# Kernel tuning notes

Hardware: AMD Instinct MI355X
Metric: run time of the kernel (lower is better)

## Reference

```python
import jax, jax.numpy as jnp
import numpy as np


def _depthwise3x3(x_nhwc, w):
    # w: (3, 3, 1, C) — depthwise conv, padding=1, matches torch Conv2d(groups=C)
    return jax.lax.conv_general_dilated(
        x_nhwc, w, window_strides=(1, 1), padding='SAME',
        dimension_numbers=('NHWC', 'HWIO', 'NHWC'),
        feature_group_count=x_nhwc.shape[-1])


def _stripe_attn(q, k, v, lepe_w, B, H, W, nh, hd, ss, axis, scale):
    # q/k/v: (B, H, W, nh*hd); axis 0 = horizontal stripes, 1 = vertical
    pad_h = (-H) % ss if axis == 0 else 0
    pad_w = (-W) % ss if axis == 1 else 0
    if pad_h or pad_w:
        pad = ((0, 0), (0, pad_h), (0, pad_w), (0, 0))
        q, k, v = jnp.pad(q, pad), jnp.pad(k, pad), jnp.pad(v, pad)
    Hp, Wp = q.shape[1], q.shape[2]
    lepe = _depthwise3x3(v, lepe_w)  # (B, Hp, Wp, nh*hd)

    if axis == 0:
        nS = Hp // ss
        def to_win(t):  # -> (B*nS*Wp, nh, ss, hd)
            t = t.reshape(B, nS, ss, Wp, nh, hd)
            return t.transpose(0, 1, 3, 4, 2, 5).reshape(B * nS * Wp, nh, ss, hd)
    else:
        nS = Wp // ss
        def to_win(t):  # -> (B*Hp*nS, nh, ss, hd)
            t = t.reshape(B, Hp, nS, ss, nh, hd)
            return t.transpose(0, 1, 2, 4, 3, 5).reshape(B * Hp * nS, nh, ss, hd)

    qw, kw, vw, lw = to_win(q), to_win(k), to_win(v), to_win(lepe)
    attn = jax.nn.softmax(jnp.einsum('wnqd,wnkd->wnqk', qw, kw) / scale, axis=-1)
    out = jnp.einsum('wnqk,wnkd->wnqd', attn, vw) + lw  # (Wnum, nh, ss, hd)

    if axis == 0:
        out = out.transpose(0, 2, 1, 3).reshape(B, nS, Wp, ss, nh * hd)
        out = out.transpose(0, 1, 3, 2, 4).reshape(B, Hp, Wp, nh * hd)
    else:
        out = out.transpose(0, 2, 1, 3).reshape(B, Hp, nS, ss, nh * hd)
        out = out.reshape(B, Hp, Wp, nh * hd)
    return out[:, :H, :W, :].reshape(B, H * W, nh * hd)


def setup_inputs() -> dict:
    key = jax.random.key(0)
    ks = jax.random.split(key, 6)
    B, H, W, dim, n_heads, ss = 8, 64, 64, 512, 16, 8
    half = dim // 2
    x = jax.random.normal(ks[0], (B, H * W, dim), dtype=jnp.float32)
    w_qkv = jax.random.normal(ks[1], (3 * dim, dim), dtype=jnp.float32) * 0.02
    w_proj = jax.random.normal(ks[2], (dim, dim), dtype=jnp.float32) * 0.02
    b_proj = jnp.zeros((dim,), dtype=jnp.float32)
    lepe_h_w = jax.random.normal(ks[3], (3, 3, 1, half), dtype=jnp.float32) * 0.1
    lepe_v_w = jax.random.normal(ks[4], (3, 3, 1, half), dtype=jnp.float32) * 0.1
    return {"x": x, "w_qkv": w_qkv, "w_proj": w_proj, "b_proj": b_proj,
            "lepe_h_w": lepe_h_w, "lepe_v_w": lepe_v_w, "H": H, "W": W}


def reference(x, w_qkv, w_proj, b_proj, lepe_h_w, lepe_v_w, H, W):
    B, L, C = x.shape
    n_heads, ss = 16, 8
    hd = C // n_heads
    scale = float(np.sqrt(hd))
    qkv = x @ w_qkv.T  # (B, L, 3C)
    q, k, v = jnp.split(qkv, 3, axis=-1)
    q = q.reshape(B, H, W, C)
    k = k.reshape(B, H, W, C)
    v = v.reshape(B, H, W, C)
    half = C // 2
    nh_h = n_heads // 2
    nh_v = n_heads - nh_h
    out_h = _stripe_attn(q[..., :half], k[..., :half], v[..., :half],
                         lepe_h_w, B, H, W, nh_h, hd, ss, axis=0, scale=scale)
    out_v = _stripe_attn(q[..., half:], k[..., half:], v[..., half:],
                         lepe_v_w, B, H, W, nh_v, hd, ss, axis=1, scale=scale)
    out = jnp.concatenate([out_h, out_v], axis=-1)
    return out @ w_proj.T + b_proj
```

## Files before the change

kernel.cpp:

```cpp
#include <hip/hip_runtime.h>
#include <hip/hip_bf16.h>
#include <stdint.h>

typedef _Float16 half2v __attribute__((ext_vector_type(2)));
typedef _Float16 half8v __attribute__((ext_vector_type(8)));
typedef uint32_t u32x4  __attribute__((ext_vector_type(4)));
typedef float    f32x4  __attribute__((ext_vector_type(4)));

__device__ __forceinline__ unsigned short f2h(float f) {
  _Float16 h = (_Float16)f;
  return __builtin_bit_cast(unsigned short, h);
}
__device__ __forceinline__ half2v bch2(uint32_t u) {
  return __builtin_bit_cast(half2v, u);
}
__device__ __forceinline__ uint32_t pkrtz_u32(float a, float b) {
  return __builtin_bit_cast(uint32_t, __builtin_amdgcn_cvt_pkrtz(a, b));
}

__device__ __forceinline__ int qkv_idx(int half, int b, int n, int h, int w) {
  int idx = half * 8388608 + (b * 8 + n) * 131072;
  idx += (half == 0) ? ((h >> 3) * 16384 + w * 256 + (h & 7) * 32)
                     : (h * 2048 + w * 32);
  return idx;
}

#define GLOAD_LDS16(gsrc, lbase)                                          \
  __builtin_amdgcn_global_load_lds(                                       \
      (const __attribute__((address_space(1))) uint32_t*)(gsrc),          \
      (__attribute__((address_space(3))) uint32_t*)(lbase), 16, 0, 0)

__global__ __launch_bounds__(256) void cvt_f32_f16(const float* __restrict__ in,
                                                   unsigned short* __restrict__ out,
                                                   int n4) {
  int i = blockIdx.x * 256 + threadIdx.x;
  if (i >= n4) return;
  float4 f = reinterpret_cast<const float4*>(in)[i];
  ushort4 u;
  u.x = f2h(f.x); u.y = f2h(f.y); u.z = f2h(f.z); u.w = f2h(f.w);
  reinterpret_cast<ushort4*>(out)[i] = u;
}

template<int MODE>
__global__ __launch_bounds__(512, 2) void gemm_bt(
    const unsigned short* __restrict__ A,
    const unsigned short* __restrict__ B,
    unsigned short* __restrict__ Cq,
    float* __restrict__ Cf,
    const float* __restrict__ bias,
    int M, int N, int K)
{
  __shared__ unsigned short As[4][256 * 32];
  __shared__ unsigned short Bs[4][256 * 32];
  const int tid  = threadIdx.x;
  const int gn   = N >> 8;
  const int cpx  = gridDim.x >> 3;
  const int bid  = blockIdx.x;
  const int wgid = (bid & 7) * cpx + (bid >> 3);
  const int m0   = (wgid / gn) * 256;
  const int n0   = (wgid % gn) * 256;
  const int wave = tid >> 6, lane = tid & 63;
  const int wr  = wave >> 2;
  const int wcn = wave & 3;
  const int sr = tid >> 2;
  const int sc = ((tid & 3) ^ ((tid >> 3) & 3)) * 8;
  const size_t aBase0 = (size_t)(m0 + sr) * K + sc;
  const size_t aBase1 = (size_t)(m0 + 128 + sr) * K + sc;
  const size_t bBase0 = (size_t)(n0 + sr) * K + sc;
  const size_t bBase1 = (size_t)(n0 + 128 + sr) * K + sc;
  char* ldsA = (char*)(&As[0][0]) + (tid & ~63) * 16;
  char* ldsB = (char*)(&Bs[0][0]) + (tid & ~63) * 16;

#define STAGE_TILE(bsel, kofs)                                      \
  do {                                                              \
    GLOAD_LDS16(A + aBase0 + (kofs), ldsA + (bsel) * 16384);        \
    GLOAD_LDS16(A + aBase1 + (kofs), ldsA + (bsel) * 16384 + 8192); \
    GLOAD_LDS16(B + bBase0 + (kofs), ldsB + (bsel) * 16384);        \
    GLOAD_LDS16(B + bBase1 + (kofs), ldsB + (bsel) * 16384 + 8192); \
  } while (0)

  STAGE_TILE(0, 0);
  STAGE_TILE(1, 32);
  STAGE_TILE(2, 64);

  f32x4 acc[8][4];
  const f32x4 zero = {0.f, 0.f, 0.f, 0.f};
  #pragma unroll
  for (int i = 0; i < 8; ++i)
    #pragma unroll
    for (int j = 0; j < 4; ++j) acc[i][j] = zero;

  const int lr   = lane & 15;
  const int slot = (lane >> 4) ^ ((lr >> 1) & 3);

  auto compute = [&](const unsigned short* Asb, const unsigned short* Bsb) {
    half8v bf[4];
    #pragma unroll
    for (int j = 0; j < 4; ++j)
      bf[j] = *reinterpret_cast<const half8v*>(Bsb + (wcn * 64 + j * 16 + lr) * 32 + slot * 8);
    half8v af[8];
    #pragma unroll
    for (int i = 0; i < 8; ++i)
      af[i] = *reinterpret_cast<const half8v*>(Asb + (wr * 128 + i * 16 + lr) * 32 + slot * 8);
    __builtin_amdgcn_s_setprio(1);
    #pragma unroll
    for (int i = 0; i < 8; ++i)
      #pragma unroll
      for (int j = 0; j < 4; ++j)
        acc[i][j] = __builtin_amdgcn_mfma_f32_16x16x32_f16(bf[j], af[i], acc[i][j], 0, 0, 0);
    __builtin_amdgcn_s_setprio(0);
  };

  const int nt = K >> 5;
  for (int t = 0; t < nt; ++t) {
    if (t + 3 < nt) STAGE_TILE((t + 3) & 3, (t + 3) * 32);
    if (t < nt - 3)       asm volatile("s_waitcnt vmcnt(12)" ::: "memory");
    else if (t == nt - 3) asm volatile("s_waitcnt vmcnt(8)"  ::: "memory");
    else if (t == nt - 2) asm volatile("s_waitcnt vmcnt(4)"  ::: "memory");
    else                  asm volatile("s_waitcnt vmcnt(0)"  ::: "memory");
    __builtin_amdgcn_s_barrier();
    __builtin_amdgcn_sched_barrier(0);
    compute(&As[t & 3][0], &Bs[t & 3][0]);
    __builtin_amdgcn_s_barrier();
    __builtin_amdgcn_sched_barrier(0);
  }
#undef STAGE_TILE

  const int cr = (lane >> 4) * 4;
  const int cc = lane & 15;

  if constexpr (MODE == 0) {
    #pragma unroll
    for (int j = 0; j < 4; ++j) {
      const int n = n0 + wcn * 64 + j * 16 + cr;
      const float4 b4 = *reinterpret_cast<const float4*>(bias + n);
      #pragma unroll
      for (int i = 0; i < 8; ++i) {
        const int m = m0 + wr * 128 + i * 16 + cc;
        float4 r;
        r.x = acc[i][j][0] + b4.x;
        r.y = acc[i][j][1] + b4.y;
        r.z = acc[i][j][2] + b4.z;
        r.w = acc[i][j][3] + b4.w;
        *reinterpret_cast<float4*>(Cf + (size_t)m * N + n) = r;
      }
    }
  } else {
    const int mb   = m0 + wr * 128;
    const int btok = mb >> 12;
    const int hr0  = (mb >> 6) & 63;
    #pragma unroll
    for (int j = 0; j < 4; ++j) {
      const int nb    = n0 + wcn * 64 + j * 16 + cr;
      const int tq    = nb >> 9;
      const int halfc = (nb >> 8) & 1;
      const int nn    = (nb & 255) >> 5;
      const int ch4   = nb & 31;
      const int headbase = tq * 16777216 + halfc * 8388608 +
                           (btok * 8 + nn) * 131072 + ch4;
      #pragma unroll
      for (int i = 0; i < 8; ++i) {
        const int hrow = hr0 + (i >> 2);
        const int wpix = (i & 3) * 16 + cc;
        const int off = halfc ? (hrow * 2048 + wpix * 32)
                              : ((hrow >> 3) * 16384 + wpix * 256 + (hrow & 7) * 32);
        uint2 r;
        r.x = pkrtz_u32(acc[i][j][0], acc[i][j][1]);
        r.y = pkrtz_u32(acc[i][j][2], acc[i][j][3]);
        *reinterpret_cast<uint2*>(Cq + headbase + off) = r;
      }
    }
  }
}

__global__ __launch_bounds__(256) void attn_lepe(
    const unsigned short* __restrict__ qkvp,
    const unsigned short* __restrict__ wlep,
    unsigned short* __restrict__ outp)
{
  const int gw   = (int)((blockIdx.x * 256 + threadIdx.x) >> 6);
  const int lane = threadIdx.x & 63;
  const int half = gw >> 14;
  const int id   = gw & 16383;
  const int b    = id >> 11;
  const int n    = (id >> 8) & 7;
  int h0, w0;
  if (half == 0) { h0 = ((id >> 5) & 7) * 8; w0 = (id & 31) * 2; }
  else           { h0 = ((id >> 3) & 31) * 2; w0 = (id & 7) * 8; }
  const int baseA = qkv_idx(half, b, n, h0, w0);
  const int dWin  = (half == 0) ? 256 : 2048;
  const int baseB = baseA + dWin;

  const int qr = lane >> 3, kr = lane & 7;
  const unsigned short* qA = qkvp + baseA + qr * 32;
  const unsigned short* kA = qkvp + 16777216 + baseA + kr * 32;
  float sA = 0.f, sB = 0.f;
  #pragma unroll
  for (int c = 0; c < 4; ++c) {
    const u32x4 qa = *reinterpret_cast<const u32x4*>(qA + c * 8);
    const u32x4 ka = *reinterpret_cast<const u32x4*>(kA + c * 8);
    const u32x4 qb = *reinterpret_cast<const u32x4*>(qA + dWin + c * 8);
    const u32x4 kb = *reinterpret_cast<const u32x4*>(kA + dWin + c * 8);
    #pragma unroll
    for (int e = 0; e < 4; ++e) {
      sA = __builtin_amdgcn_fdot2(bch2(qa[e]), bch2(ka[e]), sA, false);
      sB = __builtin_amdgcn_fdot2(bch2(qb[e]), bch2(kb[e]), sB, false);
    }
  }
  const float scl = 0.17677669529663687f;
  const float pA = __expf(sA * scl);
  const float pB = __expf(sB * scl);
  float denA = pA, denB = pB;
  denA += __shfl_xor(denA, 1); denA += __shfl_xor(denA, 2); denA += __shfl_xor(denA, 4);
  denB += __shfl_xor(denB, 1); denB += __shfl_xor(denB, 2); denB += __shfl_xor(denB, 4);
  const float aAv = pA * __builtin_amdgcn_rcpf(denA);
  const float aBv = pB * __builtin_amdgcn_rcpf(denB);
  const uint32_t adu = pkrtz_u32(aAv, aBv);

  const int dgrp = lane & 3;
  const int win  = (lane >> 2) & 1;
  const int qr2  = lane >> 3;
  const int d0   = dgrp * 8;
  const int mybase = win ? baseB : baseA;
  const unsigned short* vwin = qkvp + 33554432 + mybase;

  half2v o01 = {0,0}, o23 = {0,0}, o45 = {0,0}, o67 = {0,0};
  #pragma unroll
  for (int k = 0; k < 8; ++k) {
    const uint32_t pairw = (uint32_t)__shfl((int)adu, qr2 * 8 + k);
    const half2v ph = bch2(pairw);
    const _Float16 av = win ? ph.y : ph.x;
    const half2v ak2 = {av, av};
    const u32x4 vv = *reinterpret_cast<const u32x4*>(vwin + k * 32 + d0);
    o01 += ak2 * bch2(vv[0]);
    o23 += ak2 * bch2(vv[1]);
    o45 += ak2 * bch2(vv[2]);
    o67 += ak2 * bch2(vv[3]);
  }

  const int hq = (half == 0) ? (h0 + qr2) : (h0 + win);
  const int wq = (half == 0) ? (w0 + win) : (w0 + qr2);
  const unsigned short* vplane = qkvp + 33554432;
  const unsigned short* wl = wlep + half * 2304 + n * 32 + d0;
  half2v l01 = {0,0}, l23 = {0,0}, l45 = {0,0}, l67 = {0,0};
  #pragma unroll
  for (int dy = -1; dy <= 1; ++dy) {
    #pragma unroll
    for (int dx = -1; dx <= 1; ++dx) {
      const int hh = hq + dy, ww = wq + dx;
      u32x4 vv = {0u, 0u, 0u, 0u};
      if ((unsigned)hh < 64u && (unsigned)ww < 64u)
        vv = *reinterpret_cast<const u32x4*>(vplane + qkv_idx(half, b, n, hh, ww) + d0);
      const u32x4 wt = *reinterpret_cast<const u32x4*>(wl + ((dy + 1) * 3 + dx + 1) * 256);
      l01 += bch2(wt[0]) * bch2(vv[0]);
      l23 += bch2(wt[1]) * bch2(vv[1]);
      l45 += bch2(wt[2]) * bch2(vv[2]);
      l67 += bch2(wt[3]) * bch2(vv[3]);
    }
  }

  const int m = b * 4096 + hq * 64 + wq;
  const int chan0 = half * 256 + n * 32;
  u32x4 r;
  r[0] = __builtin_bit_cast(uint32_t, (half2v)(o01 + l01));
  r[1] = __builtin_bit_cast(uint32_t, (half2v)(o23 + l23));
  r[2] = __builtin_bit_cast(uint32_t, (half2v)(o45 + l45));
  r[3] = __builtin_bit_cast(uint32_t, (half2v)(o67 + l67));
  *reinterpret_cast<u32x4*>(outp + (size_t)m * 512 + chan0 + d0) = r;
}

extern "C" void kernel_launch(void* const* d_in, const int* in_sizes, int n_in,
                              void* d_out, int out_size, void* d_ws, size_t ws_size,
                              hipStream_t stream) {
  const float* x      = (const float*)d_in[0];
  const float* w_qkv  = (const float*)d_in[1];
  const float* w_proj = (const float*)d_in[2];
  const float* b_proj = (const float*)d_in[3];
  const float* lepe_h = (const float*)d_in[4];
  const float* lepe_v = (const float*)d_in[5];
  float* out = (float*)d_out;

  char* ws = (char*)d_ws;
  unsigned short* qkv_p   = (unsigned short*)ws;
  unsigned short* xh      = (unsigned short*)(ws + 100663296);
  unsigned short* wqkv_h  = (unsigned short*)(ws + 134217728);
  unsigned short* wproj_h = (unsigned short*)(ws + 135790592);
  unsigned short* wlep_h  = (unsigned short*)(ws + 136314880);

  cvt_f32_f16<<<16384, 256, 0, stream>>>(x, xh, 4194304);
  cvt_f32_f16<<<768,   256, 0, stream>>>(w_qkv, wqkv_h, 196608);
  cvt_f32_f16<<<256,   256, 0, stream>>>(w_proj, wproj_h, 65536);
  cvt_f32_f16<<<3,     256, 0, stream>>>(lepe_h, wlep_h, 576);
  cvt_f32_f16<<<3,     256, 0, stream>>>(lepe_v, wlep_h + 2304, 576);

  gemm_bt<1><<<768, 512, 0, stream>>>(
      xh, wqkv_h, qkv_p, nullptr, nullptr, 32768, 1536, 512);

  attn_lepe<<<8192, 256, 0, stream>>>(qkv_p, wlep_h, xh);

  gemm_bt<0><<<256, 512, 0, stream>>>(
      xh, wproj_h, nullptr, out, b_proj, 32768, 512, 512);
}
```

Before: 192.9 us.

## Restructure GEMM into K=64 double-buffered 8-phase pipeline with interleaved loads

Replaces the 4-stage K=32 LDS ring in both GEMMs with a 2-buffer K=64 tile scheme. Global-to-LDS loads for A and B are staggered across eight barrier-separated phases that alternate LDS fragment reads with 16-MFMA bursts, and K is fixed at compile time to 512. The goal is to overlap loads with MFMA work more evenly and to halve the number of outer iterations and waitcnt barriers. In exchange there are many more barriers per iteration, the swizzle and staging logic is more complex, and the kernel only works for K=512.

```diff
diff --git a/kernel.cpp b/kernel.cpp
--- a/kernel.cpp
+++ b/kernel.cpp
@@ -42,16 +42,18 @@
 }
 
 template<int MODE>
-__global__ __launch_bounds__(512, 2) void gemm_bt(
+__global__ __launch_bounds__(512, 2) void gemm8(
     const unsigned short* __restrict__ A,
-    const unsigned short* __restrict__ B,
+    const unsigned short* __restrict__ Bm,
     unsigned short* __restrict__ Cq,
     float* __restrict__ Cf,
     const float* __restrict__ bias,
-    int M, int N, int K)
+    int M, int N)
 {
-  __shared__ unsigned short As[4][256 * 32];
-  __shared__ unsigned short Bs[4][256 * 32];
+  constexpr int K = 512;
+  constexpr int NIT = 4;
+  __shared__ unsigned short As[2][256 * 64];
+  __shared__ unsigned short Bs[2][256 * 64];
   const int tid  = threadIdx.x;
   const int gn   = N >> 8;
   const int cpx  = gridDim.x >> 3;
@@ -62,26 +64,35 @@
   const int wave = tid >> 6, lane = tid & 63;
   const int wr  = wave >> 2;
   const int wcn = wave & 3;
-  const int sr = tid >> 2;
-  const int sc = ((tid & 3) ^ ((tid >> 3) & 3)) * 8;
-  const size_t aBase0 = (size_t)(m0 + sr) * K + sc;
-  const size_t aBase1 = (size_t)(m0 + 128 + sr) * K + sc;
-  const size_t bBase0 = (size_t)(n0 + sr) * K + sc;
-  const size_t bBase1 = (size_t)(n0 + 128 + sr) * K + sc;
+
+  const int srow = tid >> 3;
+  const int schk = ((tid & 7) ^ (srow & 7)) * 8;
+  const size_t aSrc = (size_t)(m0 + srow) * K + schk;
+  const size_t bSrc = (size_t)(n0 + srow) * K + schk;
   char* ldsA = (char*)(&As[0][0]) + (tid & ~63) * 16;
   char* ldsB = (char*)(&Bs[0][0]) + (tid & ~63) * 16;
 
-#define STAGE_TILE(bsel, kofs)                                      \
-  do {                                                              \
-    GLOAD_LDS16(A + aBase0 + (kofs), ldsA + (bsel) * 16384);        \
-    GLOAD_LDS16(A + aBase1 + (kofs), ldsA + (bsel) * 16384 + 8192); \
-    GLOAD_LDS16(B + bBase0 + (kofs), ldsB + (bsel) * 16384);        \
-    GLOAD_LDS16(B + bBase1 + (kofs), ldsB + (bsel) * 16384 + 8192); \
-  } while (0)
-
-  STAGE_TILE(0, 0);
-  STAGE_TILE(1, 32);
-  STAGE_TILE(2, 64);
+#define STAGE_A8(b, kt)                                                     \
+  do {                                                                      \
+    GLOAD_LDS16(A + aSrc + (size_t)(kt) * 64,             ldsA + (b) * 32768);         \
+    GLOAD_LDS16(A + aSrc + (size_t)64 * K + (kt) * 64,    ldsA + (b) * 32768 + 8192);  \
+    GLOAD_LDS16(A + aSrc + (size_t)128 * K + (kt) * 64,   ldsA + (b) * 32768 + 16384); \
+    GLOAD_LDS16(A + aSrc + (size_t)192 * K + (kt) * 64,   ldsA + (b) * 32768 + 24576); \
+  } while (0)
+#define STAGE_B8(b, kt)                                                     \
+  do {                                                                      \
+    GLOAD_LDS16(Bm + bSrc + (size_t)(kt) * 64,            ldsB + (b) * 32768);         \
+    GLOAD_LDS16(Bm + bSrc + (size_t)64 * K + (kt) * 64,   ldsB + (b) * 32768 + 8192);  \
+    GLOAD_LDS16(Bm + bSrc + (size_t)128 * K + (kt) * 64,  ldsB + (b) * 32768 + 16384); \
+    GLOAD_LDS16(Bm + bSrc + (size_t)192 * K + (kt) * 64,  ldsB + (b) * 32768 + 24576); \
+  } while (0)
+#define BARS                                                                \
+  __builtin_amdgcn_s_barrier();                                             \
+  __builtin_amdgcn_sched_barrier(0)
+
+  STAGE_A8(0, 0);
+  STAGE_B8(0, 0);
+  STAGE_B8(1, 1);
 
   f32x4 acc[8][4];
   const f32x4 zero = {0.f, 0.f, 0.f, 0.f};
@@ -90,41 +101,99 @@
     #pragma unroll
     for (int j = 0; j < 4; ++j) acc[i][j] = zero;
 
-  const int lr   = lane & 15;
-  const int slot = (lane >> 4) ^ ((lr >> 1) & 3);
-
-  auto compute = [&](const unsigned short* Asb, const unsigned short* Bsb) {
-    half8v bf[4];
-    #pragma unroll
-    for (int j = 0; j < 4; ++j)
-      bf[j] = *reinterpret_cast<const half8v*>(Bsb + (wcn * 64 + j * 16 + lr) * 32 + slot * 8);
-    half8v af[8];
-    #pragma unroll
-    for (int i = 0; i < 8; ++i)
-      af[i] = *reinterpret_cast<const half8v*>(Asb + (wr * 128 + i * 16 + lr) * 32 + slot * 8);
-    __builtin_amdgcn_s_setprio(1);
-    #pragma unroll
-    for (int i = 0; i < 8; ++i)
-      #pragma unroll
-      for (int j = 0; j < 4; ++j)
-        acc[i][j] = __builtin_amdgcn_mfma_f32_16x16x32_f16(bf[j], af[i], acc[i][j], 0, 0, 0);
-    __builtin_amdgcn_s_setprio(0);
-  };
-
-  const int nt = K >> 5;
-  for (int t = 0; t < nt; ++t) {
-    if (t + 3 < nt) STAGE_TILE((t + 3) & 3, (t + 3) * 32);
-    if (t < nt - 3)       asm volatile("s_waitcnt vmcnt(12)" ::: "memory");
-    else if (t == nt - 3) asm volatile("s_waitcnt vmcnt(8)"  ::: "memory");
-    else if (t == nt - 2) asm volatile("s_waitcnt vmcnt(4)"  ::: "memory");
-    else                  asm volatile("s_waitcnt vmcnt(0)"  ::: "memory");
-    __builtin_amdgcn_s_barrier();
-    __builtin_amdgcn_sched_barrier(0);
-    compute(&As[t & 3][0], &Bs[t & 3][0]);
-    __builtin_amdgcn_s_barrier();
-    __builtin_amdgcn_sched_barrier(0);
-  }
-#undef STAGE_TILE
+  const int lr  = lane & 15;
+  const int kg  = lane >> 4;
+  const int ck0 = kg ^ (lr & 7);
+
+  asm volatile("s_waitcnt vmcnt(4)" ::: "memory");
+  BARS;
+
+#define LD_AF(buf, mg, ks)                                                  \
+  do {                                                                      \
+    const unsigned short* ap = &As[buf][0] +                                \
+        (wr * 128 + (mg) * 64 + lr) * 64 + (((ks) ? (ck0 ^ 4) : ck0)) * 8;  \
+    af[0] = *(const half8v*)(ap);                                           \
+    af[1] = *(const half8v*)(ap + 1024);                                    \
+    af[2] = *(const half8v*)(ap + 2048);                                    \
+    af[3] = *(const half8v*)(ap + 3072);                                    \
+  } while (0)
+#define LD_BF(buf, ks)                                                      \
+  do {                                                                      \
+    const unsigned short* bp = &Bs[buf][0] +                                \
+        (wcn * 64 + lr) * 64 + (((ks) ? (ck0 ^ 4) : ck0)) * 8;              \
+    bf[0] = *(const half8v*)(bp);                                           \
+    bf[1] = *(const half8v*)(bp + 1024);                                    \
+    bf[2] = *(const half8v*)(bp + 2048);                                    \
+    bf[3] = *(const half8v*)(bp + 3072);                                    \
+  } while (0)
+#define MROW(mg, i)                                                         \
+  acc[(mg)*4+(i)][0] = __builtin_amdgcn_mfma_f32_16x16x32_f16(bf[0], af[i], acc[(mg)*4+(i)][0], 0, 0, 0); \
+  acc[(mg)*4+(i)][1] = __builtin_amdgcn_mfma_f32_16x16x32_f16(bf[1], af[i], acc[(mg)*4+(i)][1], 0, 0, 0); \
+  acc[(mg)*4+(i)][2] = __builtin_amdgcn_mfma_f32_16x16x32_f16(bf[2], af[i], acc[(mg)*4+(i)][2], 0, 0, 0); \
+  acc[(mg)*4+(i)][3] = __builtin_amdgcn_mfma_f32_16x16x32_f16(bf[3], af[i], acc[(mg)*4+(i)][3], 0, 0, 0);
+#define MFMA16(mg)                                                          \
+  do {                                                                      \
+    __builtin_amdgcn_s_setprio(1);                                          \
+    MROW(mg, 0); MROW(mg, 1); MROW(mg, 2); MROW(mg, 3);                     \
+    __builtin_amdgcn_s_setprio(0);                                          \
+  } while (0)
+
+  for (int it2 = 0; it2 < NIT; ++it2) {
+    const bool more = (it2 + 1 < NIT);
+    const int keven = 2 * it2;
+    half8v af[4], bf[4];
+    LD_BF(0, 0); LD_AF(0, 0, 0);
+    STAGE_A8(1, keven + 1);
+    BARS;
+    MFMA16(0);
+    BARS;
+    LD_AF(0, 1, 0);
+    BARS;
+    MFMA16(1);
+    BARS;
+    LD_BF(0, 1); LD_AF(0, 0, 1);
+    BARS;
+    MFMA16(0);
+    BARS;
+    LD_AF(0, 1, 1);
+    if (more) {
+      STAGE_B8(0, keven + 2);
+      asm volatile("s_waitcnt vmcnt(4)" ::: "memory");
+    } else {
+      asm volatile("s_waitcnt vmcnt(0)" ::: "memory");
+    }
+    BARS;
+    MFMA16(1);
+    BARS;
+    LD_BF(1, 0); LD_AF(1, 0, 0);
+    if (more) STAGE_A8(0, keven + 2);
+    BARS;
+    MFMA16(0);
+    BARS;
+    LD_AF(1, 1, 0);
+    BARS;
+    MFMA16(1);
+    BARS;
+    LD_BF(1, 1); LD_AF(1, 0, 1);
+    BARS;
+    MFMA16(0);
+    BARS;
+    LD_AF(1, 1, 1);
+    if (more) {
+      STAGE_B8(1, keven + 3);
+      asm volatile("s_waitcnt vmcnt(4)" ::: "memory");
+    }
+    BARS;
+    MFMA16(1);
+    BARS;
+  }
+#undef STAGE_A8
+#undef STAGE_B8
+#undef LD_AF
+#undef LD_BF
+#undef MROW
+#undef MFMA16
+#undef BARS
 
   const int cr = (lane >> 4) * 4;
   const int cc = lane & 15;
@@ -293,11 +362,11 @@
   cvt_f32_f16<<<3,     256, 0, stream>>>(lepe_h, wlep_h, 576);
   cvt_f32_f16<<<3,     256, 0, stream>>>(lepe_v, wlep_h + 2304, 576);
 
-  gemm_bt<1><<<768, 512, 0, stream>>>(
-      xh, wqkv_h, qkv_p, nullptr, nullptr, 32768, 1536, 512);
+  gemm8<1><<<768, 512, 0, stream>>>(
+      xh, wqkv_h, qkv_p, nullptr, nullptr, 32768, 1536);
 
   attn_lepe<<<8192, 256, 0, stream>>>(qkv_p, wlep_h, xh);
 
-  gemm_bt<0><<<256, 512, 0, stream>>>(
-      xh, wproj_h, nullptr, out, b_proj, 32768, 512, 512);
-}
+  gemm8<0><<<256, 512, 0, stream>>>(
+      xh, wproj_h, nullptr, out, b_proj, 32768, 512);
+}
```

After: 175.6 us. -9.0%, faster.
